# Kernel optimization log

Hardware: AMD Instinct MI355X
Metric: run time of the kernel (lower is better)

## Reference

```python
import jax, jax.numpy as jnp
import numpy as np

NUM_HEADS = 8
GROUP = 16
LN_EPS = 1e-5

def _star_relu(x, scale, bias):
    return scale * jnp.square(jax.nn.relu(x)) + bias

def _layernorm(x, w, b):
    mu = x.mean(-1, keepdims=True)
    var = jnp.mean(jnp.square(x - mu), -1, keepdims=True)
    return (x - mu) / jnp.sqrt(var + LN_EPS) * w + b

def _attention(x, qkv_w, proj_w, proj_b, pa_scale, pa_bias, lf_w, lf_b, hf_w, hf_b, lf_gamma, hf_gamma):
    B, N, C = x.shape
    hd = C // NUM_HEADS
    detail = _star_relu(x, pa_scale, pa_bias)
    lf = jnp.tanh(detail @ lf_w.T + lf_b)                      # (B,N,H)
    hf = jax.nn.softplus(detail @ hf_w.T + hf_b)
    hf_sq = jnp.square(hf)
    hf = 2.0 * hf_sq / (hf_sq + 0.3678)
    lf = jnp.repeat(lf, hd, axis=-1)                           # (B,N,C): per-head value repeated across head_dim
    hf = jnp.repeat(hf, hd, axis=-1)
    qkv = (x @ qkv_w.T).reshape(B, N, 3, NUM_HEADS, hd).transpose(2, 0, 3, 1, 4)
    q, k, v = qkv[0], qkv[1], qkv[2]
    q = q * (hd ** -0.5)
    attn = jax.nn.softmax(jnp.einsum('bhqd,bhkd->bhqk', q, k), axis=-1)
    attn_out = jnp.einsum('bhqk,bhkd->bhqd', attn, v).transpose(0, 2, 1, 3).reshape(B, N, C)
    value_tokens = v.transpose(0, 2, 1, 3).reshape(B, N, C)
    high_res = value_tokens - attn_out
    attn_out = attn_out + attn_out * lf * lf_gamma + hf * high_res * hf_gamma
    return attn_out @ proj_w.T + proj_b

def _freq_scale(x, rw1_w, rw1_scale, rw1_bias, rw2_w, freq_w):
    # x: (B,C,H,W); freq_w: (num_filters, C//group, base_size, base_size//2+1) == rfft grid
    B, C, H, W = x.shape
    xf = jnp.fft.rfft2(x, axes=(2, 3), norm='ortho')           # (B,C,fh,fw) complex
    pooled = x.mean(axis=(2, 3))                               # (B,C)
    h = _star_relu(pooled @ rw1_w.T, rw1_scale, rw1_bias)
    routing = jnp.tanh((h @ rw2_w.T).reshape(B, GROUP, -1))    # (B,g,f)
    fh, fw = xf.shape[2], xf.shape[3]
    dyn = jnp.einsum('bgf,fchw->bgchw', routing, freq_w).reshape(B, C, fh, fw)
    xf = xf * dyn
    return jnp.fft.irfft2(xf, s=(H, W), axes=(2, 3), norm='ortho')

def _forward(x, norm1_w, norm1_b, qkv_w, proj_w, proj_b, pa_scale, pa_bias, lf_w, lf_b, hf_w, hf_b,
             lf_gamma, hf_gamma, fs1_rw1_w, fs1_rw1_scale, fs1_rw1_bias, fs1_rw2_w, fs1_fw, gamma_1,
             norm2_w, norm2_b, fc1_w, fc1_b, fc2_w, fc2_b, fs2_rw1_w, fs2_rw1_scale, fs2_rw1_bias,
             fs2_rw2_w, fs2_fw, gamma_2):
    B, C, H, W = x.shape
    tokens = x.reshape(B, C, H * W).transpose(0, 2, 1)         # nchw -> nlc
    att_tokens = _attention(_layernorm(tokens, norm1_w, norm1_b),
                            qkv_w, proj_w, proj_b, pa_scale, pa_bias,
                            lf_w, lf_b, hf_w, hf_b, lf_gamma, hf_gamma)
    att_feat = att_tokens.transpose(0, 2, 1).reshape(B, C, H, W)
    att_feat = _freq_scale(att_feat, fs1_rw1_w, fs1_rw1_scale, fs1_rw1_bias, fs1_rw2_w, fs1_fw) + att_feat
    att_tokens = att_feat.reshape(B, C, H * W).transpose(0, 2, 1)
    tokens = tokens + gamma_1 * att_tokens
    h = _layernorm(tokens, norm2_w, norm2_b)
    mlp_tokens = jax.nn.gelu(h @ fc1_w.T + fc1_b, approximate=False) @ fc2_w.T + fc2_b
    mlp_feat = mlp_tokens.transpose(0, 2, 1).reshape(B, C, H, W)
    mlp_feat = _freq_scale(mlp_feat, fs2_rw1_w, fs2_rw1_scale, fs2_rw1_bias, fs2_rw2_w, fs2_fw) + mlp_feat
    mlp_tokens = mlp_feat.reshape(B, C, H * W).transpose(0, 2, 1)
    tokens = tokens + gamma_2 * mlp_tokens
    return tokens.transpose(0, 2, 1).reshape(B, C, H, W)

def setup_inputs() -> dict:
    key = jax.random.key(0)
    ks = jax.random.split(key, 16)
    B, C, H, W = 16, 512, 32, 32
    heads, group, nf, bs = 8, 16, 4, 32
    hid_rw = int(C * 0.125)
    hid_mlp = int(C * 4.0)
    bfs = bs // 2 + 1
    d = {}
    d['x'] = jax.random.normal(ks[0], (B, C, H, W), jnp.float32)
    d['norm1_w'] = jnp.ones((C,), jnp.float32); d['norm1_b'] = jnp.zeros((C,), jnp.float32)
    d['qkv_w'] = jax.random.normal(ks[1], (3 * C, C), jnp.float32) * 0.02
    d['proj_w'] = jax.random.normal(ks[2], (C, C), jnp.float32) * 0.02
    d['proj_b'] = jnp.zeros((C,), jnp.float32)
    d['pa_scale'] = jnp.ones((1,), jnp.float32); d['pa_bias'] = jnp.zeros((1,), jnp.float32)
    d['lf_w'] = jax.random.normal(ks[3], (heads, C), jnp.float32) * 0.02
    d['lf_b'] = jnp.zeros((heads,), jnp.float32)
    d['hf_w'] = jax.random.normal(ks[4], (heads, C), jnp.float32) * 0.02
    d['hf_b'] = jnp.zeros((heads,), jnp.float32)
    d['lf_gamma'] = 1e-5 * jnp.ones((C,), jnp.float32)
    d['hf_gamma'] = 1e-5 * jnp.ones((C,), jnp.float32)
    d['fs1_rw1_w'] = jax.random.normal(ks[5], (hid_rw, C), jnp.float32) * 0.02
    d['fs1_rw1_scale'] = jnp.ones((1,), jnp.float32); d['fs1_rw1_bias'] = jnp.zeros((1,), jnp.float32)
    d['fs1_rw2_w'] = jax.random.normal(ks[6], (group * nf, hid_rw), jnp.float32) * 0.02
    d['fs1_fw'] = jax.random.normal(ks[7], (nf, C // group, bs, bfs), jnp.float32) * 1e-5
    d['gamma_1'] = 1e-4 * jnp.ones((C,), jnp.float32)
    d['norm2_w'] = jnp.ones((C,), jnp.float32); d['norm2_b'] = jnp.zeros((C,), jnp.float32)
    d['fc1_w'] = jax.random.normal(ks[8], (hid_mlp, C), jnp.float32) * 0.02
    d['fc1_b'] = jnp.zeros((hid_mlp,), jnp.float32)
    d['fc2_w'] = jax.random.normal(ks[9], (C, hid_mlp), jnp.float32) * 0.02
    d['fc2_b'] = jnp.zeros((C,), jnp.float32)
    d['fs2_rw1_w'] = jax.random.normal(ks[10], (hid_rw, C), jnp.float32) * 0.02
    d['fs2_rw1_scale'] = jnp.ones((1,), jnp.float32); d['fs2_rw1_bias'] = jnp.zeros((1,), jnp.float32)
    d['fs2_rw2_w'] = jax.random.normal(ks[11], (group * nf, hid_rw), jnp.float32) * 0.02
    d['fs2_fw'] = jax.random.normal(ks[12], (nf, C // group, bs, bfs), jnp.float32) * 1e-5
    d['gamma_2'] = 1e-4 * jnp.ones((C,), jnp.float32)
    return d

def reference(x, norm1_w, norm1_b, qkv_w, proj_w, proj_b, pa_scale, pa_bias, lf_w, lf_b, hf_w, hf_b,
              lf_gamma, hf_gamma, fs1_rw1_w, fs1_rw1_scale, fs1_rw1_bias, fs1_rw2_w, fs1_fw, gamma_1,
              norm2_w, norm2_b, fc1_w, fc1_b, fc2_w, fc2_b, fs2_rw1_w, fs2_rw1_scale, fs2_rw1_bias,
              fs2_rw2_w, fs2_fw, gamma_2):
    return _forward(x, norm1_w, norm1_b, qkv_w, proj_w, proj_b, pa_scale, pa_bias, lf_w, lf_b, hf_w, hf_b,
                    lf_gamma, hf_gamma, fs1_rw1_w, fs1_rw1_scale, fs1_rw1_bias, fs1_rw2_w, fs1_fw, gamma_1,
                    norm2_w, norm2_b, fc1_w, fc1_b, fc2_w, fc2_b, fs2_rw1_w, fs2_rw1_scale, fs2_rw1_bias,
                    fs2_rw2_w, fs2_fw, gamma_2)
```

## Files before the change

kernel.cpp:

```cpp
#include <hip/hip_runtime.h>
#include <cstdint>
#include <cstddef>

#define B_   16
#define C_   512
#define N_   1024
#define M_   (B_*N_)
#define NH_  8
#define HD_  64
#define C3_  1536
#define CH_  2048

typedef __attribute__((ext_vector_type(8))) short bf16x8;
typedef __attribute__((ext_vector_type(4))) float f32x4;
typedef __attribute__((ext_vector_type(4))) unsigned short u16x4;

__device__ __forceinline__ unsigned short f2bf(float f) {
  union { float f; unsigned u; } v; v.f = f;
  unsigned r = v.u + 0x7fffu + ((v.u >> 16) & 1u);
  return (unsigned short)(r >> 16);
}
__device__ __forceinline__ float bf2f(unsigned short h) {
  union { unsigned u; float f; } v; v.u = ((unsigned)h) << 16;
  return v.f;
}
__device__ __forceinline__ unsigned f2u(float f) {
  union { float f; unsigned u; } v; v.f = f; return v.u;
}

__global__ __launch_bounds__(256) void k_f2b4(
    const float* __restrict__ s0, unsigned short* __restrict__ d0,
    const float* __restrict__ s1, unsigned short* __restrict__ d1,
    const float* __restrict__ s2, unsigned short* __restrict__ d2,
    const float* __restrict__ s3, unsigned short* __restrict__ d3) {
  int blk = blockIdx.x, t = threadIdx.x;
  const float* s; unsigned short* d; int off;
  if (blk < 3072)      { s = s0; d = d0; off = blk * 256; }
  else if (blk < 4096) { s = s1; d = d1; off = (blk - 3072) * 256; }
  else if (blk < 8192) { s = s2; d = d2; off = (blk - 4096) * 256; }
  else                 { s = s3; d = d3; off = (blk - 8192) * 256; }
  int i = off + t;
  d[i] = f2bf(s[i]);
}

__global__ __launch_bounds__(256) void k_twid(unsigned short* __restrict__ gtab) {
  int idx = blockIdx.x * 256 + threadIdx.x;
  if (idx >= 6400) return;
  int tab = idx / 1280, rem = idx % 1280;
  int i = rem / 40, j = rem % 40;
  float v = 0.f;
  if (j < 32) {
    float th = 0.19634954084936207f * (float)((i * j) & 31);
    float s, c;
    __sincosf(th, &s, &c);
    if (tab == 0) v = c;
    else if (tab == 1) v = s;
    else if (tab == 2) v = -s;
    else {
      float wg = (j == 0 || j == 16) ? 1.f : 2.f;
      if (j >= 17) wg = 0.f;
      v = (tab == 3) ? wg * c : -wg * s;
    }
  }
  gtab[idx] = f2bf(v);
}

template<bool WITH>
__global__ __launch_bounds__(256) void k_lnt(const float* __restrict__ src,
    const float* __restrict__ w, const float* __restrict__ bia,
    const float* __restrict__ lfw, const float* __restrict__ lfb,
    const float* __restrict__ hfw, const float* __restrict__ hfb,
    const float* __restrict__ pa_s, const float* __restrict__ pa_b,
    unsigned short* __restrict__ lnout, float* __restrict__ lfout,
    float* __restrict__ hfout) {
  __shared__ unsigned short s[512 * 34];
  const int t = threadIdx.x, wv = t >> 6, l = t & 63;
  const int n0 = blockIdx.x * 32, b = blockIdx.y;
  const int cl = t >> 3;
  const int nn = (t & 7) * 4;
  #pragma unroll
  for (int k = 0; k < 16; ++k) {
    int c = k * 32 + cl;
    float4 v = *(const float4*)&src[(size_t)(b * C_ + c) * N_ + n0 + nn];
    s[c * 34 + nn]     = f2bf(v.x);
    s[c * 34 + nn + 1] = f2bf(v.y);
    s[c * 34 + nn + 2] = f2bf(v.z);
    s[c * 34 + nn + 3] = f2bf(v.w);
  }
  __syncthreads();
  float wv8[8], bv8[8];
  #pragma unroll
  for (int k = 0; k < 8; ++k) { wv8[k] = w[l + 64 * k]; bv8[k] = bia[l + 64 * k]; }
  float ps = 1.f, pb = 0.f;
  if (WITH) { ps = pa_s[0]; pb = pa_b[0]; }
  for (int ri = 0; ri < 8; ++ri) {
    const int n = wv * 8 + ri;
    const int row = b * N_ + n0 + n;
    float v[8];
    #pragma unroll
    for (int k = 0; k < 8; ++k) v[k] = bf2f(s[(l + 64 * k) * 34 + n]);
    float sm = 0.f, q = 0.f;
    #pragma unroll
    for (int k = 0; k < 8; ++k) { sm += v[k]; q += v[k] * v[k]; }
    #pragma unroll
    for (int off = 1; off < 64; off <<= 1) { sm += __shfl_xor(sm, off); q += __shfl_xor(q, off); }
    float mu = sm * (1.f / 512.f);
    float var = q * (1.f / 512.f) - mu * mu;
    float rstd = rsqrtf(var + 1e-5f);
    float ln[8];
    #pragma unroll
    for (int k = 0; k < 8; ++k) ln[k] = (v[k] - mu) * rstd * wv8[k] + bv8[k];
    #pragma unroll
    for (int k = 0; k < 8; ++k)
      lnout[(size_t)row * C_ + l + 64 * k] = f2bf(ln[k]);
    if (WITH) {
      float d[8];
      #pragma unroll
      for (int k = 0; k < 8; ++k) { float r = fmaxf(ln[k], 0.f); d[k] = ps * r * r + pb; }
      float lacc[8], hacc[8];
      #pragma unroll
      for (int h = 0; h < 8; ++h) {
        float la = 0.f, ha = 0.f;
        #pragma unroll
        for (int k = 0; k < 8; ++k) {
          la += d[k] * lfw[h * C_ + l + 64 * k];
          ha += d[k] * hfw[h * C_ + l + 64 * k];
        }
        lacc[h] = la; hacc[h] = ha;
      }
      #pragma unroll
      for (int h = 0; h < 8; ++h)
        #pragma unroll
        for (int off = 1; off < 64; off <<= 1) {
          lacc[h] += __shfl_xor(lacc[h], off);
          hacc[h] += __shfl_xor(hacc[h], off);
        }
      float lv = lacc[0], hv = hacc[0];
      #pragma unroll
      for (int h = 1; h < 8; ++h) { if (l == h) { lv = lacc[h]; hv = hacc[h]; } }
      if (l < 8) {
        lfout[(size_t)row * 8 + l] = tanhf(lv + lfb[l]);
        float z = hv + hfb[l];
        float sp = (z > 15.f) ? z : log1pf(__expf(z));
        float s2 = sp * sp;
        hfout[(size_t)row * 8 + l] = 2.f * s2 / (s2 + 0.3678f);
      }
    }
  }
}

template<int EPI>
__global__ __launch_bounds__(256) void k_gemm(const unsigned short* __restrict__ A,
    const unsigned short* __restrict__ Bt, const float* __restrict__ bias,
    void* __restrict__ outv, unsigned short* __restrict__ vtg, int Nn, int K) {
  __shared__ __align__(16) unsigned short Asm[128 * 40];
  __shared__ __align__(16) unsigned short Bsm[128 * 40];
  const int t = threadIdx.x, w = t >> 6, l = t & 63;
  const int lane15 = l & 15, quad = l >> 4;
  const int n0 = blockIdx.x * 128, m0 = blockIdx.y * 128;
  const int wm = w >> 1, wn = w & 1;
  f32x4 acc[4][4];
  #pragma unroll
  for (int i = 0; i < 4; ++i)
    #pragma unroll
    for (int j = 0; j < 4; ++j) acc[i][j] = (f32x4){0.f, 0.f, 0.f, 0.f};
  const int sr = t >> 2, sc = (t & 3) * 8;
  const unsigned short* Ab = A + (size_t)(m0 + sr) * K + sc;
  const unsigned short* Bb = Bt + (size_t)(n0 + sr) * K + sc;
  const size_t rstep = (size_t)64 * K;
  bf16x8 ga0 = *(const bf16x8*)Ab;
  bf16x8 ga1 = *(const bf16x8*)(Ab + rstep);
  bf16x8 gb0 = *(const bf16x8*)Bb;
  bf16x8 gb1 = *(const bf16x8*)(Bb + rstep);
  for (int k0 = 0; k0 < K; k0 += 32) {
    __syncthreads();
    *(bf16x8*)&Asm[sr * 40 + sc] = ga0;
    *(bf16x8*)&Asm[(sr + 64) * 40 + sc] = ga1;
    *(bf16x8*)&Bsm[sr * 40 + sc] = gb0;
    *(bf16x8*)&Bsm[(sr + 64) * 40 + sc] = gb1;
    __syncthreads();
    if (k0 + 32 < K) {
      ga0 = *(const bf16x8*)(Ab + k0 + 32);
      ga1 = *(const bf16x8*)(Ab + rstep + k0 + 32);
      gb0 = *(const bf16x8*)(Bb + k0 + 32);
      gb1 = *(const bf16x8*)(Bb + rstep + k0 + 32);
    }
    bf16x8 af[4], bg[4];
    #pragma unroll
    for (int i = 0; i < 4; ++i)
      af[i] = *(const bf16x8*)&Asm[(wm * 64 + i * 16 + lane15) * 40 + quad * 8];
    #pragma unroll
    for (int i = 0; i < 4; ++i)
      bg[i] = *(const bf16x8*)&Bsm[(wn * 64 + i * 16 + lane15) * 40 + quad * 8];
    #pragma unroll
    for (int i = 0; i < 4; ++i)
      #pragma unroll
      for (int j = 0; j < 4; ++j)
        acc[i][j] = __builtin_amdgcn_mfma_f32_16x16x32_bf16(af[i], bg[j], acc[i][j], 0, 0, 0);
  }
  #pragma unroll
  for (int i = 0; i < 4; ++i) {
    int grow = m0 + wm * 64 + i * 16 + quad * 4;
    int bq = grow >> 10, nq = grow & 1023;
    #pragma unroll
    for (int j = 0; j < 4; ++j) {
      int gcol = n0 + wn * 64 + j * 16 + lane15;
      float bs = (EPI == 0) ? 0.f : bias[gcol];
      if (EPI == 1 || EPI == 3) {
        float4 o = make_float4(acc[i][j][0] + bs, acc[i][j][1] + bs,
                               acc[i][j][2] + bs, acc[i][j][3] + bs);
        *(float4*)&((float*)outv)[((size_t)(bq * C_ + gcol) << 10) + nq] = o;
      } else if (EPI == 0) {
        u16x4 pv;
        #pragma unroll
        for (int r = 0; r < 4; ++r) {
          unsigned short hv = f2bf(acc[i][j][r]);
          pv[r] = hv;
          ((unsigned short*)outv)[(size_t)(grow + r) * Nn + gcol] = hv;
        }
        if (gcol >= 1024)
          *(u16x4*)&vtg[((size_t)(bq * C_ + gcol - 1024) << 10) + nq] = pv;
      } else {
        #pragma unroll
        for (int r = 0; r < 4; ++r) {
          float vv = acc[i][j][r] + bs;
          float e = __builtin_amdgcn_exp2f(-(2.302118073f * vv +
                                             0.1029455568f * vv * vv * vv));
          float g = vv * __builtin_amdgcn_rcpf(1.f + e);
          ((unsigned short*)outv)[(size_t)(grow + r) * Nn + gcol] = f2bf(g);
        }
      }
    }
  }
}

__global__ __launch_bounds__(256) void k_flash(const unsigned short* __restrict__ qkv,
    const unsigned short* __restrict__ vtg, const float* __restrict__ lf,
    const float* __restrict__ hf, const float* __restrict__ lgam,
    const float* __restrict__ hgam, unsigned short* __restrict__ y) {
  const int t = threadIdx.x, w = t >> 6, l = t & 63;
  const int lane15 = l & 15, quad = l >> 4;
  const int q0 = blockIdx.x * 64;
  const int h = blockIdx.y, b = blockIdx.z;
  __shared__ __align__(16) unsigned short kt[128 * 72];
  __shared__ __align__(16) unsigned short vt[64 * 136];
  __shared__ __align__(16) unsigned short pl[4][16 * 72];

  bf16x8 aq0, aq1;
  {
    const unsigned short* qp = qkv + (size_t)(b * N_ + q0 + w * 16 + lane15) * C3_ + h * 64 + quad * 8;
    bf16x8 r0 = *(const bf16x8*)qp;
    bf16x8 r1 = *(const bf16x8*)(qp + 32);
    #pragma unroll
    for (int i = 0; i < 8; ++i) {
      aq0[i] = (short)f2bf(0.1803368801111713f * bf2f((unsigned short)r0[i]));
      aq1[i] = (short)f2bf(0.1803368801111713f * bf2f((unsigned short)r1[i]));
    }
  }
  f32x4 O[4];
  #pragma unroll
  for (int i = 0; i < 4; ++i) O[i] = (f32x4){0.f, 0.f, 0.f, 0.f};
  float lsum = 0.f;

  const int sr = t >> 3;
  const int sc = (t & 7) * 8;
  const unsigned short* kb = qkv + (size_t)(b * N_ + sr) * C3_ + 512 + h * 64 + sc;
  const unsigned short* vb = vtg + (size_t)((b * NH_ + h) * HD_ + sr) * N_ + sc;
  bf16x8 gk0 = *(const bf16x8*)kb;
  bf16x8 gk1 = *(const bf16x8*)(kb + (size_t)32 * C3_);
  bf16x8 gk2 = *(const bf16x8*)(kb + (size_t)64 * C3_);
  bf16x8 gk3 = *(const bf16x8*)(kb + (size_t)96 * C3_);
  bf16x8 gv0 = *(const bf16x8*)vb;
  bf16x8 gv1 = *(const bf16x8*)(vb + 64);
  bf16x8 gv2 = *(const bf16x8*)(vb + 32 * N_);
  bf16x8 gv3 = *(const bf16x8*)(vb + 32 * N_ + 64);

  for (int kti = 0; kti < 8; ++kti) {
    __syncthreads();
    *(bf16x8*)&kt[sr * 72 + sc] = gk0;
    *(bf16x8*)&kt[(sr + 32) * 72 + sc] = gk1;
    *(bf16x8*)&kt[(sr + 64) * 72 + sc] = gk2;
    *(bf16x8*)&kt[(sr + 96) * 72 + sc] = gk3;
    *(bf16x8*)&vt[sr * 136 + sc] = gv0;
    *(bf16x8*)&vt[sr * 136 + 64 + sc] = gv1;
    *(bf16x8*)&vt[(sr + 32) * 136 + sc] = gv2;
    *(bf16x8*)&vt[(sr + 32) * 136 + 64 + sc] = gv3;
    __syncthreads();
    if (kti < 7) {
      const unsigned short* kn = kb + (size_t)((kti + 1) * 128) * C3_;
      const unsigned short* vn = vb + (kti + 1) * 128;
      gk0 = *(const bf16x8*)kn;
      gk1 = *(const bf16x8*)(kn + (size_t)32 * C3_);
      gk2 = *(const bf16x8*)(kn + (size_t)64 * C3_);
      gk3 = *(const bf16x8*)(kn + (size_t)96 * C3_);
      gv0 = *(const bf16x8*)vn;
      gv1 = *(const bf16x8*)(vn + 64);
      gv2 = *(const bf16x8*)(vn + 32 * N_);
      gv3 = *(const bf16x8*)(vn + 32 * N_ + 64);
    }

    #pragma unroll
    for (int half = 0; half < 2; ++half) {
      f32x4 S[4];
      #pragma unroll
      for (int nt = 0; nt < 4; ++nt) {
        const int nrow = half * 64 + nt * 16 + lane15;
        bf16x8 ak0 = *(const bf16x8*)&kt[nrow * 72 + quad * 8];
        bf16x8 ak1 = *(const bf16x8*)&kt[nrow * 72 + 32 + quad * 8];
        f32x4 z = (f32x4){0.f, 0.f, 0.f, 0.f};
        z = __builtin_amdgcn_mfma_f32_16x16x32_bf16(ak0, aq0, z, 0, 0, 0);
        z = __builtin_amdgcn_mfma_f32_16x16x32_bf16(ak1, aq1, z, 0, 0, 0);
        S[nt] = z;
      }
      #pragma unroll
      for (int nt = 0; nt < 4; ++nt)
        #pragma unroll
        for (int r = 0; r < 4; ++r) {
          float pv = __builtin_amdgcn_exp2f(S[nt][r]);
          S[nt][r] = pv;
          lsum += pv;
        }
      #pragma unroll
      for (int nt = 0; nt < 4; ++nt) {
        unsigned lo = __builtin_amdgcn_perm(f2u(S[nt][1]), f2u(S[nt][0]), 0x07060302u);
        unsigned hi = __builtin_amdgcn_perm(f2u(S[nt][3]), f2u(S[nt][2]), 0x07060302u);
        uint2 pk = make_uint2(lo, hi);
        *(uint2*)&pl[w][lane15 * 72 + nt * 16 + quad * 4] = pk;
      }
      #pragma unroll
      for (int nc = 0; nc < 2; ++nc) {
        bf16x8 ap = *(const bf16x8*)&pl[w][lane15 * 72 + nc * 32 + quad * 8];
        #pragma unroll
        for (int dt = 0; dt < 4; ++dt) {
          bf16x8 bv = *(const bf16x8*)&vt[(dt * 16 + lane15) * 136 + half * 64 + nc * 32 + quad * 8];
          O[dt] = __builtin_amdgcn_mfma_f32_16x16x32_bf16(ap, bv, O[dt], 0, 0, 0);
        }
      }
    }
  }

  lsum += __shfl_xor(lsum, 16);
  lsum += __shfl_xor(lsum, 32);
  float inv = 1.f / lsum;
  float invr[4], lfr[4], hfr[4];
  #pragma unroll
  for (int r = 0; r < 4; ++r) {
    invr[r] = __shfl(inv, quad * 4 + r);
    int grow = b * N_ + q0 + w * 16 + quad * 4 + r;
    lfr[r] = lf[grow * 8 + h];
    hfr[r] = hf[grow * 8 + h];
  }
  const size_t rowb = (size_t)(b * N_ + q0 + w * 16 + quad * 4);
  #pragma unroll
  for (int dt = 0; dt < 4; ++dt) {
    int cc = h * 64 + dt * 16 + lane15;
    float lg = lgam[cc], hg = hgam[cc];
    #pragma unroll
    for (int r = 0; r < 4; ++r) {
      float a = O[dt][r] * invr[r];
      float vval = bf2f(qkv[(rowb + r) * C3_ + 1024 + cc]);
      float res = a + a * lfr[r] * lg + hfr[r] * (vval - a) * hg;
      y[(rowb + r) * C_ + cc] = f2bf(res);
    }
  }
}

__global__ __launch_bounds__(256) void k_pool(const float* __restrict__ feat,
                                              float* __restrict__ pooled) {
  int row = blockIdx.x * 4 + (threadIdx.x >> 6);
  int l = threadIdx.x & 63;
  const float4* p = (const float4*)(feat + (size_t)row * N_);
  float4 a = p[l], b4 = p[l + 64], c4 = p[l + 128], d4 = p[l + 192];
  float s = a.x + a.y + a.z + a.w + b4.x + b4.y + b4.z + b4.w +
            c4.x + c4.y + c4.z + c4.w + d4.x + d4.y + d4.z + d4.w;
  #pragma unroll
  for (int off = 1; off < 64; off <<= 1) s += __shfl_xor(s, off);
  if (l == 0) pooled[row] = s * (1.f / 1024.f);
}

__global__ __launch_bounds__(256) void k_routing(const float* __restrict__ pooled,
    const float* __restrict__ rw1, const float* __restrict__ rw1s,
    const float* __restrict__ rw1b, const float* __restrict__ rw2,
    float* __restrict__ routing) {
  const int b = blockIdx.x, t = threadIdx.x;
  __shared__ float plds[512];
  __shared__ float tile[64][65];
  __shared__ float hl[64];
  plds[t] = pooled[b * 512 + t];
  plds[t + 256] = pooled[b * 512 + t + 256];
  __syncthreads();
  float acc = 0.f;
  for (int c0 = 0; c0 < 512; c0 += 64) {
    #pragma unroll
    for (int kk = 0; kk < 16; ++kk) {
      int idx = kk * 256 + t;
      tile[idx >> 6][idx & 63] = rw1[(size_t)(idx >> 6) * 512 + c0 + (idx & 63)];
    }
    __syncthreads();
    if (t < 64) {
      #pragma unroll
      for (int i = 0; i < 64; ++i) acc += plds[c0 + i] * tile[t][i];
    }
    __syncthreads();
  }
  if (t < 64) {
    float r = fmaxf(acc, 0.f);
    hl[t] = rw1s[0] * r * r + rw1b[0];
  }
  __syncthreads();
  if (t < 64) {
    float r2 = 0.f;
    #pragma unroll
    for (int j = 0; j < 64; ++j) r2 += hl[j] * rw2[(size_t)t * 64 + j];
    routing[b * 64 + t] = tanhf(r2);
  }
}

__global__ __launch_bounds__(256) void k_freq(const float* __restrict__ feat,
    const float* __restrict__ routing, const float* __restrict__ fwtab,
    const unsigned short* __restrict__ gtab, const float* __restrict__ res,
    const float* __restrict__ gamma, float* __restrict__ outp) {
  const int c = blockIdx.x, b = blockIdx.y, t = threadIdx.x;
  const int g = c >> 5, cc = c & 31;
  const int w = t >> 6, l = t & 63;
  const int lane15 = l & 15, quad = l >> 4;
  const int mt = w & 1, nt = w >> 1;
  __shared__ __align__(16) unsigned short Xbf[32 * 40];
  __shared__ __align__(16) float p[32 * 36];
  __shared__ __align__(16) unsigned short Tabs[6400];
  __shared__ __align__(16) unsigned short pl1r[32 * 40], pl1i[32 * 40];
  __shared__ __align__(16) unsigned short pl2r[32 * 40], pl2i[32 * 40];
  __shared__ __align__(16) unsigned short pl3r[32 * 40], pl3i[32 * 40];
  __shared__ float Ms[1024];
  const size_t base = (size_t)(b * C_ + c) * N_;

  {
    float4 v = ((const float4*)(feat + base))[t];
    int hh = t >> 3, w4 = (t & 7) * 4;
    *(float4*)&p[hh * 36 + w4] = v;
    u16x4 xb = { f2bf(v.x), f2bf(v.y), f2bf(v.z), f2bf(v.w) };
    *(u16x4*)&Xbf[hh * 40 + w4] = xb;
  }
  {
    const uint4* src = (const uint4*)gtab;
    uint4* dst = (uint4*)Tabs;
    #pragma unroll
    for (int k = 0; k < 4; ++k) {
      int o = k * 256 + t;
      if (o < 800) dst[o] = src[o];
    }
  }
  {
    float r0 = routing[b * 64 + g * 4 + 0];
    float r1 = routing[b * 64 + g * 4 + 1];
    float r2 = routing[b * 64 + g * 4 + 2];
    float r3 = routing[b * 64 + g * 4 + 3];
    const float* fb = fwtab + (size_t)cc * 544;
    #pragma unroll
    for (int k = 0; k < 4; ++k) {
      int o = k * 256 + t;
      int fh = o >> 5, fw = o & 31;
      float mv = 0.f;
      if (fw < 17) {
        int fi = fh * 17 + fw;
        mv = (r0 * fb[fi] + r1 * fb[17408 + fi] + r2 * fb[34816 + fi] +
              r3 * fb[52224 + fi]) * (1.f / 1024.f);
      }
      Ms[o] = mv;
    }
  }
  __syncthreads();

  const unsigned short* Tc  = Tabs;
  const unsigned short* Ts  = Tabs + 1280;
  const unsigned short* Tsn = Tabs + 2560;
  const unsigned short* Tcw = Tabs + 3840;
  const unsigned short* Tsw = Tabs + 5120;
  const int arow = (mt * 16 + lane15) * 40 + quad * 8;
  const int brow = (nt * 16 + lane15) * 40 + quad * 8;
  const int prow = (nt * 16 + lane15) * 40 + mt * 16 + quad * 4;
  const f32x4 zz = (f32x4){0.f, 0.f, 0.f, 0.f};

  {
    bf16x8 aX = *(const bf16x8*)&Xbf[arow];
    bf16x8 bC = *(const bf16x8*)&Tc[brow];
    bf16x8 bS = *(const bf16x8*)&Tsn[brow];
    f32x4 re = __builtin_amdgcn_mfma_f32_16x16x32_bf16(aX, bC, zz, 0, 0, 0);
    f32x4 im = __builtin_amdgcn_mfma_f32_16x16x32_bf16(aX, bS, zz, 0, 0, 0);
    uint2 pr = make_uint2(__builtin_amdgcn_perm(f2u(re[1]), f2u(re[0]), 0x07060302u),
                          __builtin_amdgcn_perm(f2u(re[3]), f2u(re[2]), 0x07060302u));
    uint2 pi = make_uint2(__builtin_amdgcn_perm(f2u(im[1]), f2u(im[0]), 0x07060302u),
                          __builtin_amdgcn_perm(f2u(im[3]), f2u(im[2]), 0x07060302u));
    *(uint2*)&pl1r[prow] = pr;
    *(uint2*)&pl1i[prow] = pi;
  }
  __syncthreads();
  {
    bf16x8 aC = *(const bf16x8*)&Tc[arow];
    bf16x8 aS = *(const bf16x8*)&Ts[arow];
    bf16x8 aN = *(const bf16x8*)&Tsn[arow];
    bf16x8 bR = *(const bf16x8*)&pl1r[brow];
    bf16x8 bI = *(const bf16x8*)&pl1i[brow];
    f32x4 er = __builtin_amdgcn_mfma_f32_16x16x32_bf16(aC, bR, zz, 0, 0, 0);
    er = __builtin_amdgcn_mfma_f32_16x16x32_bf16(aS, bI, er, 0, 0, 0);
    f32x4 ei = __builtin_amdgcn_mfma_f32_16x16x32_bf16(aC, bI, zz, 0, 0, 0);
    ei = __builtin_amdgcn_mfma_f32_16x16x32_bf16(aN, bR, ei, 0, 0, 0);
    #pragma unroll
    for (int r = 0; r < 4; ++r) {
      float mk = Ms[(mt * 16 + quad * 4 + r) * 32 + nt * 16 + lane15];
      er[r] *= mk; ei[r] *= mk;
    }
    uint2 pr = make_uint2(__builtin_amdgcn_perm(f2u(er[1]), f2u(er[0]), 0x07060302u),
                          __builtin_amdgcn_perm(f2u(er[3]), f2u(er[2]), 0x07060302u));
    uint2 pi = make_uint2(__builtin_amdgcn_perm(f2u(ei[1]), f2u(ei[0]), 0x07060302u),
                          __builtin_amdgcn_perm(f2u(ei[3]), f2u(ei[2]), 0x07060302u));
    *(uint2*)&pl2r[prow] = pr;
    *(uint2*)&pl2i[prow] = pi;
  }
  __syncthreads();
  {
    bf16x8 aR = *(const bf16x8*)&pl2r[arow];
    bf16x8 aI = *(const bf16x8*)&pl2i[arow];
    bf16x8 bC = *(const bf16x8*)&Tc[brow];
    bf16x8 bS = *(const bf16x8*)&Ts[brow];
    bf16x8 bN = *(const bf16x8*)&Tsn[brow];
    f32x4 zr = __builtin_amdgcn_mfma_f32_16x16x32_bf16(aR, bC, zz, 0, 0, 0);
    zr = __builtin_amdgcn_mfma_f32_16x16x32_bf16(aI, bN, zr, 0, 0, 0);
    f32x4 zi = __builtin_amdgcn_mfma_f32_16x16x32_bf16(aI, bC, zz, 0, 0, 0);
    zi = __builtin_amdgcn_mfma_f32_16x16x32_bf16(aR, bS, zi, 0, 0, 0);
    uint2 pr = make_uint2(__builtin_amdgcn_perm(f2u(zr[1]), f2u(zr[0]), 0x07060302u),
                          __builtin_amdgcn_perm(f2u(zr[3]), f2u(zr[2]), 0x07060302u));
    uint2 pi = make_uint2(__builtin_amdgcn_perm(f2u(zi[1]), f2u(zi[0]), 0x07060302u),
                          __builtin_amdgcn_perm(f2u(zi[3]), f2u(zi[2]), 0x07060302u));
    *(uint2*)&pl3r[prow] = pr;
    *(uint2*)&pl3i[prow] = pi;
  }
  __syncthreads();
  {
    bf16x8 aC = *(const bf16x8*)&Tcw[arow];
    bf16x8 aS = *(const bf16x8*)&Tsw[arow];
    bf16x8 bR = *(const bf16x8*)&pl3r[brow];
    bf16x8 bI = *(const bf16x8*)&pl3i[brow];
    f32x4 y = __builtin_amdgcn_mfma_f32_16x16x32_bf16(aC, bR, zz, 0, 0, 0);
    y = __builtin_amdgcn_mfma_f32_16x16x32_bf16(aS, bI, y, 0, 0, 0);
    int hh = nt * 16 + lane15, w0 = mt * 16 + quad * 4;
    float4 fp = *(const float4*)&p[hh * 36 + w0];
    float4 rp = *(const float4*)&res[base + hh * 32 + w0];
    float gv = gamma[c];
    float4 o = make_float4(rp.x + gv * (y[0] + fp.x), rp.y + gv * (y[1] + fp.y),
                           rp.z + gv * (y[2] + fp.z), rp.w + gv * (y[3] + fp.w));
    *(float4*)&outp[base + hh * 32 + w0] = o;
  }
}

extern "C" void kernel_launch(void* const* d_in, const int* in_sizes, int n_in,
                              void* d_out, int out_size, void* d_ws, size_t ws_size,
                              hipStream_t stream) {
  (void)in_sizes; (void)n_in; (void)out_size; (void)ws_size;
  const float* x      = (const float*)d_in[0];
  const float* n1w    = (const float*)d_in[1];
  const float* n1b    = (const float*)d_in[2];
  const float* qkv_w  = (const float*)d_in[3];
  const float* proj_w = (const float*)d_in[4];
  const float* proj_b = (const float*)d_in[5];
  const float* pa_s   = (const float*)d_in[6];
  const float* pa_b   = (const float*)d_in[7];
  const float* lf_w   = (const float*)d_in[8];
  const float* lf_b   = (const float*)d_in[9];
  const float* hf_w   = (const float*)d_in[10];
  const float* hf_b   = (const float*)d_in[11];
  const float* lf_g   = (const float*)d_in[12];
  const float* hf_g   = (const float*)d_in[13];
  const float* f1rw1w = (const float*)d_in[14];
  const float* f1rw1s = (const float*)d_in[15];
  const float* f1rw1b = (const float*)d_in[16];
  const float* f1rw2w = (const float*)d_in[17];
  const float* f1fw   = (const float*)d_in[18];
  const float* gamma1 = (const float*)d_in[19];
  const float* n2w    = (const float*)d_in[20];
  const float* n2b    = (const float*)d_in[21];
  const float* fc1w   = (const float*)d_in[22];
  const float* fc1b   = (const float*)d_in[23];
  const float* fc2w   = (const float*)d_in[24];
  const float* fc2b   = (const float*)d_in[25];
  const float* f2rw1w = (const float*)d_in[26];
  const float* f2rw1s = (const float*)d_in[27];
  const float* f2rw1b = (const float*)d_in[28];
  const float* f2rw2w = (const float*)d_in[29];
  const float* f2fw   = (const float*)d_in[30];
  const float* gamma2 = (const float*)d_in[31];

  char* ws = (char*)d_ws;
  float*          tokens = (float*)(ws + 0);
  float*          f1buf  = (float*)(ws + 33554432ULL);
  float*          f2buf  = (float*)(ws + 67108864ULL);
  unsigned short* regA   = (unsigned short*)(ws + 134217728ULL);
  unsigned short* abuf   = (unsigned short*)(ws + 201326592ULL);
  float*          lfbuf  = (float*)(ws + 218103808ULL);
  float*          hfbuf  = (float*)(ws + 218628096ULL);
  float*          pooled = (float*)(ws + 219152384ULL);
  float*          routing= (float*)(ws + 219185152ULL);
  unsigned short* wq     = (unsigned short*)(ws + 219189248ULL);
  unsigned short* wp     = (unsigned short*)(ws + 220762112ULL);
  unsigned short* w1     = (unsigned short*)(ws + 221286400ULL);
  unsigned short* w2     = (unsigned short*)(ws + 223383552ULL);
  unsigned short* gtab   = (unsigned short*)(ws + 225480704ULL);
  unsigned short* vtg    = (unsigned short*)f1buf;

  k_f2b4<<<12288, 256, 0, stream>>>(qkv_w, wq, proj_w, wp, fc1w, w1, fc2w, w2);
  k_twid<<<25, 256, 0, stream>>>(gtab);

  k_lnt<true><<<dim3(32, 16), 256, 0, stream>>>(x, n1w, n1b, lf_w, lf_b, hf_w, hf_b,
                                                pa_s, pa_b, abuf, lfbuf, hfbuf);
  k_gemm<0><<<dim3(12, 128), 256, 0, stream>>>(abuf, wq, n1b, regA, vtg, C3_, C_);
  k_flash<<<dim3(16, 8, 16), 256, 0, stream>>>(regA, vtg, lfbuf, hfbuf, lf_g, hf_g, abuf);
  k_gemm<1><<<dim3(4, 128), 256, 0, stream>>>(abuf, wp, proj_b, f2buf, nullptr, C_, C_);
  k_pool<<<2048, 256, 0, stream>>>(f2buf, pooled);
  k_routing<<<16, 256, 0, stream>>>(pooled, f1rw1w, f1rw1s, f1rw1b, f1rw2w, routing);
  k_freq<<<dim3(512, 16), 256, 0, stream>>>(f2buf, routing, f1fw, gtab, x, gamma1, tokens);
  k_lnt<false><<<dim3(32, 16), 256, 0, stream>>>(tokens, n2w, n2b, nullptr, nullptr,
                                                 nullptr, nullptr, nullptr, nullptr,
                                                 abuf, nullptr, nullptr);
  k_gemm<2><<<dim3(16, 128), 256, 0, stream>>>(abuf, w1, fc1b, regA, nullptr, CH_, C_);
  k_gemm<3><<<dim3(4, 128), 256, 0, stream>>>(regA, w2, fc2b, f2buf, nullptr, C_, CH_);
  k_pool<<<2048, 256, 0, stream>>>(f2buf, pooled);
  k_routing<<<16, 256, 0, stream>>>(pooled, f2rw1w, f2rw1s, f2rw1b, f2rw2w, routing);
  k_freq<<<dim3(512, 16), 256, 0, stream>>>(f2buf, routing, f2fw, gtab, tokens, gamma2,
                                            (float*)d_out);
}
```

Before: 519.1 us.

## Use direct global-to-LDS loads and XCD-aware block remapping in GEMM and flash attention

GEMM and flash-attention tile staging now uses global_load_lds, which writes global data straight into LDS instead of going through registers. The LDS padding is replaced by unpadded tiles, with an XOR swizzle in flash attention. Blocks are remapped with XCD-aware ordering so neighbouring tiles share an L2. Flash now processes 128 queries per block with 64-key tiles, uses s_setprio around MFMA sections and sets occupancy bounds. The register prefetch double-buffering is removed, so load latency is no longer overlapped, and the unpadded GEMM LDS layout may cause bank conflicts.

```diff
diff --git a/kernel.cpp b/kernel.cpp
--- a/kernel.cpp
+++ b/kernel.cpp
@@ -27,6 +27,11 @@
 __device__ __forceinline__ unsigned f2u(float f) {
   union { float f; unsigned u; } v; v.f = f; return v.u;
 }
+
+#define GL16(gp, lp) \
+  __builtin_amdgcn_global_load_lds( \
+      (const __attribute__((address_space(1))) unsigned int*)(const void*)(gp), \
+      (__attribute__((address_space(3))) unsigned int*)(void*)(lp), 16, 0, 0)
 
 __global__ __launch_bounds__(256) void k_f2b4(
     const float* __restrict__ s0, unsigned short* __restrict__ d0,
@@ -152,46 +157,44 @@
 template<int EPI>
 __global__ __launch_bounds__(256) void k_gemm(const unsigned short* __restrict__ A,
     const unsigned short* __restrict__ Bt, const float* __restrict__ bias,
-    void* __restrict__ outv, unsigned short* __restrict__ vtg, int Nn, int K) {
-  __shared__ __align__(16) unsigned short Asm[128 * 40];
-  __shared__ __align__(16) unsigned short Bsm[128 * 40];
+    void* __restrict__ outv, unsigned short* __restrict__ vtg, int Nn, int K, int nx) {
+  __shared__ __align__(16) unsigned short Asm[128 * 32];
+  __shared__ __align__(16) unsigned short Bsm[128 * 32];
   const int t = threadIdx.x, w = t >> 6, l = t & 63;
   const int lane15 = l & 15, quad = l >> 4;
-  const int n0 = blockIdx.x * 128, m0 = blockIdx.y * 128;
+  const int cpx = gridDim.x >> 3;
+  const int wgs = (blockIdx.x & 7) * cpx + (blockIdx.x >> 3);
+  const int bx = wgs % nx, by = wgs / nx;
+  const int n0 = bx * 128, m0 = by * 128;
   const int wm = w >> 1, wn = w & 1;
   f32x4 acc[4][4];
   #pragma unroll
   for (int i = 0; i < 4; ++i)
     #pragma unroll
     for (int j = 0; j < 4; ++j) acc[i][j] = (f32x4){0.f, 0.f, 0.f, 0.f};
-  const int sr = t >> 2, sc = (t & 3) * 8;
-  const unsigned short* Ab = A + (size_t)(m0 + sr) * K + sc;
-  const unsigned short* Bb = Bt + (size_t)(n0 + sr) * K + sc;
-  const size_t rstep = (size_t)64 * K;
-  bf16x8 ga0 = *(const bf16x8*)Ab;
-  bf16x8 ga1 = *(const bf16x8*)(Ab + rstep);
-  bf16x8 gb0 = *(const bf16x8*)Bb;
-  bf16x8 gb1 = *(const bf16x8*)(Bb + rstep);
+  const int srow = w * 16 + (l >> 2);
+  const int scol = (l & 3) * 8;
+  const unsigned short* gA = A + (size_t)(m0 + srow) * K + scol;
+  const unsigned short* gB = Bt + (size_t)(n0 + srow) * K + scol;
+  const size_t rk64 = (size_t)64 * K;
+  char* lA0 = (char*)Asm + w * 1024;
+  char* lA1 = (char*)Asm + 4096 + w * 1024;
+  char* lB0 = (char*)Bsm + w * 1024;
+  char* lB1 = (char*)Bsm + 4096 + w * 1024;
   for (int k0 = 0; k0 < K; k0 += 32) {
     __syncthreads();
-    *(bf16x8*)&Asm[sr * 40 + sc] = ga0;
-    *(bf16x8*)&Asm[(sr + 64) * 40 + sc] = ga1;
-    *(bf16x8*)&Bsm[sr * 40 + sc] = gb0;
-    *(bf16x8*)&Bsm[(sr + 64) * 40 + sc] = gb1;
+    GL16(gA + k0, lA0);
+    GL16(gA + k0 + rk64, lA1);
+    GL16(gB + k0, lB0);
+    GL16(gB + k0 + rk64, lB1);
     __syncthreads();
-    if (k0 + 32 < K) {
-      ga0 = *(const bf16x8*)(Ab + k0 + 32);
-      ga1 = *(const bf16x8*)(Ab + rstep + k0 + 32);
-      gb0 = *(const bf16x8*)(Bb + k0 + 32);
-      gb1 = *(const bf16x8*)(Bb + rstep + k0 + 32);
-    }
     bf16x8 af[4], bg[4];
     #pragma unroll
     for (int i = 0; i < 4; ++i)
-      af[i] = *(const bf16x8*)&Asm[(wm * 64 + i * 16 + lane15) * 40 + quad * 8];
+      af[i] = *(const bf16x8*)&Asm[(wm * 64 + i * 16 + lane15) * 32 + quad * 8];
     #pragma unroll
     for (int i = 0; i < 4; ++i)
-      bg[i] = *(const bf16x8*)&Bsm[(wn * 64 + i * 16 + lane15) * 40 + quad * 8];
+      bg[i] = *(const bf16x8*)&Bsm[(wn * 64 + i * 16 + lane15) * 32 + quad * 8];
     #pragma unroll
     for (int i = 0; i < 4; ++i)
       #pragma unroll
@@ -234,133 +237,131 @@
   }
 }
 
-__global__ __launch_bounds__(256) void k_flash(const unsigned short* __restrict__ qkv,
+__global__ __launch_bounds__(256, 4) void k_flash(const unsigned short* __restrict__ qkv,
     const unsigned short* __restrict__ vtg, const float* __restrict__ lf,
     const float* __restrict__ hf, const float* __restrict__ lgam,
     const float* __restrict__ hgam, unsigned short* __restrict__ y) {
   const int t = threadIdx.x, w = t >> 6, l = t & 63;
   const int lane15 = l & 15, quad = l >> 4;
-  const int q0 = blockIdx.x * 64;
-  const int h = blockIdx.y, b = blockIdx.z;
-  __shared__ __align__(16) unsigned short kt[128 * 72];
-  __shared__ __align__(16) unsigned short vt[64 * 136];
+  const int wg = (blockIdx.x & 7) * 128 + (blockIdx.x >> 3);
+  const int qt = wg & 7;
+  const int h = (wg >> 3) & 7;
+  const int b = wg >> 6;
+  const int q0 = qt * 128;
+
+  __shared__ __align__(16) unsigned short kt[64 * 64];
+  __shared__ __align__(16) unsigned short vt[64 * 64];
   __shared__ __align__(16) unsigned short pl[4][16 * 72];
 
-  bf16x8 aq0, aq1;
-  {
-    const unsigned short* qp = qkv + (size_t)(b * N_ + q0 + w * 16 + lane15) * C3_ + h * 64 + quad * 8;
+  bf16x8 aq[2][2];
+  #pragma unroll
+  for (int qh = 0; qh < 2; ++qh) {
+    const unsigned short* qp = qkv +
+        (size_t)(b * N_ + q0 + w * 32 + qh * 16 + lane15) * C3_ + h * 64 + quad * 8;
     bf16x8 r0 = *(const bf16x8*)qp;
     bf16x8 r1 = *(const bf16x8*)(qp + 32);
     #pragma unroll
     for (int i = 0; i < 8; ++i) {
-      aq0[i] = (short)f2bf(0.1803368801111713f * bf2f((unsigned short)r0[i]));
-      aq1[i] = (short)f2bf(0.1803368801111713f * bf2f((unsigned short)r1[i]));
-    }
-  }
-  f32x4 O[4];
-  #pragma unroll
-  for (int i = 0; i < 4; ++i) O[i] = (f32x4){0.f, 0.f, 0.f, 0.f};
-  float lsum = 0.f;
-
-  const int sr = t >> 3;
-  const int sc = (t & 7) * 8;
-  const unsigned short* kb = qkv + (size_t)(b * N_ + sr) * C3_ + 512 + h * 64 + sc;
-  const unsigned short* vb = vtg + (size_t)((b * NH_ + h) * HD_ + sr) * N_ + sc;
-  bf16x8 gk0 = *(const bf16x8*)kb;
-  bf16x8 gk1 = *(const bf16x8*)(kb + (size_t)32 * C3_);
-  bf16x8 gk2 = *(const bf16x8*)(kb + (size_t)64 * C3_);
-  bf16x8 gk3 = *(const bf16x8*)(kb + (size_t)96 * C3_);
-  bf16x8 gv0 = *(const bf16x8*)vb;
-  bf16x8 gv1 = *(const bf16x8*)(vb + 64);
-  bf16x8 gv2 = *(const bf16x8*)(vb + 32 * N_);
-  bf16x8 gv3 = *(const bf16x8*)(vb + 32 * N_ + 64);
-
-  for (int kti = 0; kti < 8; ++kti) {
+      aq[qh][0][i] = (short)f2bf(0.1803368801111713f * bf2f((unsigned short)r0[i]));
+      aq[qh][1][i] = (short)f2bf(0.1803368801111713f * bf2f((unsigned short)r1[i]));
+    }
+  }
+  f32x4 O[2][4];
+  #pragma unroll
+  for (int qh = 0; qh < 2; ++qh)
+    #pragma unroll
+    for (int i = 0; i < 4; ++i) O[qh][i] = (f32x4){0.f, 0.f, 0.f, 0.f};
+  float lsum[2] = {0.f, 0.f};
+
+  const int prow = w * 8 + (l >> 3);
+  const int csw = ((l & 7) ^ (l >> 3)) * 8;
+  const unsigned short* kg = qkv + (size_t)(b * N_ + prow) * C3_ + 512 + h * 64 + csw;
+  const unsigned short* vg = vtg + (size_t)((b * NH_ + h) * HD_ + prow) * N_ + csw;
+  char* ktb0 = (char*)kt + w * 1024;
+  char* ktb1 = (char*)kt + 4096 + w * 1024;
+  char* vtb0 = (char*)vt + w * 1024;
+  char* vtb1 = (char*)vt + 4096 + w * 1024;
+  const int swx = (lane15 & 7) * 8;
+
+  for (int kti = 0; kti < 16; ++kti) {
     __syncthreads();
-    *(bf16x8*)&kt[sr * 72 + sc] = gk0;
-    *(bf16x8*)&kt[(sr + 32) * 72 + sc] = gk1;
-    *(bf16x8*)&kt[(sr + 64) * 72 + sc] = gk2;
-    *(bf16x8*)&kt[(sr + 96) * 72 + sc] = gk3;
-    *(bf16x8*)&vt[sr * 136 + sc] = gv0;
-    *(bf16x8*)&vt[sr * 136 + 64 + sc] = gv1;
-    *(bf16x8*)&vt[(sr + 32) * 136 + sc] = gv2;
-    *(bf16x8*)&vt[(sr + 32) * 136 + 64 + sc] = gv3;
+    const unsigned short* kr = kg + (size_t)(kti * 64) * C3_;
+    GL16(kr, ktb0);
+    GL16(kr + (size_t)32 * C3_, ktb1);
+    const unsigned short* vr = vg + kti * 64;
+    GL16(vr, vtb0);
+    GL16(vr + 32 * N_, vtb1);
     __syncthreads();
-    if (kti < 7) {
-      const unsigned short* kn = kb + (size_t)((kti + 1) * 128) * C3_;
-      const unsigned short* vn = vb + (kti + 1) * 128;
-      gk0 = *(const bf16x8*)kn;
-      gk1 = *(const bf16x8*)(kn + (size_t)32 * C3_);
-      gk2 = *(const bf16x8*)(kn + (size_t)64 * C3_);
-      gk3 = *(const bf16x8*)(kn + (size_t)96 * C3_);
-      gv0 = *(const bf16x8*)vn;
-      gv1 = *(const bf16x8*)(vn + 64);
-      gv2 = *(const bf16x8*)(vn + 32 * N_);
-      gv3 = *(const bf16x8*)(vn + 32 * N_ + 64);
-    }
-
-    #pragma unroll
-    for (int half = 0; half < 2; ++half) {
+
+    #pragma unroll
+    for (int qh = 0; qh < 2; ++qh) {
       f32x4 S[4];
+      __builtin_amdgcn_s_setprio(1);
       #pragma unroll
       for (int nt = 0; nt < 4; ++nt) {
-        const int nrow = half * 64 + nt * 16 + lane15;
-        bf16x8 ak0 = *(const bf16x8*)&kt[nrow * 72 + quad * 8];
-        bf16x8 ak1 = *(const bf16x8*)&kt[nrow * 72 + 32 + quad * 8];
+        const int nrow = nt * 16 + lane15;
+        bf16x8 ak0 = *(const bf16x8*)&kt[nrow * 64 + ((quad * 8) ^ swx)];
+        bf16x8 ak1 = *(const bf16x8*)&kt[nrow * 64 + ((32 + quad * 8) ^ swx)];
         f32x4 z = (f32x4){0.f, 0.f, 0.f, 0.f};
-        z = __builtin_amdgcn_mfma_f32_16x16x32_bf16(ak0, aq0, z, 0, 0, 0);
-        z = __builtin_amdgcn_mfma_f32_16x16x32_bf16(ak1, aq1, z, 0, 0, 0);
+        z = __builtin_amdgcn_mfma_f32_16x16x32_bf16(ak0, aq[qh][0], z, 0, 0, 0);
+        z = __builtin_amdgcn_mfma_f32_16x16x32_bf16(ak1, aq[qh][1], z, 0, 0, 0);
         S[nt] = z;
       }
+      __builtin_amdgcn_s_setprio(0);
       #pragma unroll
       for (int nt = 0; nt < 4; ++nt)
         #pragma unroll
         for (int r = 0; r < 4; ++r) {
           float pv = __builtin_amdgcn_exp2f(S[nt][r]);
           S[nt][r] = pv;
-          lsum += pv;
+          lsum[qh] += pv;
         }
       #pragma unroll
       for (int nt = 0; nt < 4; ++nt) {
         unsigned lo = __builtin_amdgcn_perm(f2u(S[nt][1]), f2u(S[nt][0]), 0x07060302u);
         unsigned hi = __builtin_amdgcn_perm(f2u(S[nt][3]), f2u(S[nt][2]), 0x07060302u);
-        uint2 pk = make_uint2(lo, hi);
-        *(uint2*)&pl[w][lane15 * 72 + nt * 16 + quad * 4] = pk;
-      }
+        *(uint2*)&pl[w][lane15 * 72 + nt * 16 + quad * 4] = make_uint2(lo, hi);
+      }
+      __builtin_amdgcn_s_setprio(1);
       #pragma unroll
       for (int nc = 0; nc < 2; ++nc) {
         bf16x8 ap = *(const bf16x8*)&pl[w][lane15 * 72 + nc * 32 + quad * 8];
         #pragma unroll
         for (int dt = 0; dt < 4; ++dt) {
-          bf16x8 bv = *(const bf16x8*)&vt[(dt * 16 + lane15) * 136 + half * 64 + nc * 32 + quad * 8];
-          O[dt] = __builtin_amdgcn_mfma_f32_16x16x32_bf16(ap, bv, O[dt], 0, 0, 0);
+          const int vrow = dt * 16 + lane15;
+          bf16x8 bv = *(const bf16x8*)&vt[vrow * 64 + ((nc * 32 + quad * 8) ^ swx)];
+          O[qh][dt] = __builtin_amdgcn_mfma_f32_16x16x32_bf16(ap, bv, O[qh][dt], 0, 0, 0);
         }
       }
-    }
-  }
-
-  lsum += __shfl_xor(lsum, 16);
-  lsum += __shfl_xor(lsum, 32);
-  float inv = 1.f / lsum;
-  float invr[4], lfr[4], hfr[4];
-  #pragma unroll
-  for (int r = 0; r < 4; ++r) {
-    invr[r] = __shfl(inv, quad * 4 + r);
-    int grow = b * N_ + q0 + w * 16 + quad * 4 + r;
-    lfr[r] = lf[grow * 8 + h];
-    hfr[r] = hf[grow * 8 + h];
-  }
-  const size_t rowb = (size_t)(b * N_ + q0 + w * 16 + quad * 4);
-  #pragma unroll
-  for (int dt = 0; dt < 4; ++dt) {
-    int cc = h * 64 + dt * 16 + lane15;
-    float lg = lgam[cc], hg = hgam[cc];
+      __builtin_amdgcn_s_setprio(0);
+    }
+  }
+
+  #pragma unroll
+  for (int qh = 0; qh < 2; ++qh) {
+    float s = lsum[qh];
+    s += __shfl_xor(s, 16);
+    s += __shfl_xor(s, 32);
+    float inv = 1.f / s;
+    float invr[4], lfr[4], hfr[4];
+    const size_t rowb = (size_t)(b * N_ + q0 + w * 32 + qh * 16 + quad * 4);
     #pragma unroll
     for (int r = 0; r < 4; ++r) {
-      float a = O[dt][r] * invr[r];
-      float vval = bf2f(qkv[(rowb + r) * C3_ + 1024 + cc]);
-      float res = a + a * lfr[r] * lg + hfr[r] * (vval - a) * hg;
-      y[(rowb + r) * C_ + cc] = f2bf(res);
+      invr[r] = __shfl(inv, quad * 4 + r);
+      lfr[r] = lf[(rowb + r) * 8 + h];
+      hfr[r] = hf[(rowb + r) * 8 + h];
+    }
+    #pragma unroll
+    for (int dt = 0; dt < 4; ++dt) {
+      const int cc = h * 64 + dt * 16 + lane15;
+      const float lg = lgam[cc], hg = hgam[cc];
+      #pragma unroll
+      for (int r = 0; r < 4; ++r) {
+        float a = O[qh][dt][r] * invr[r];
+        float vval = bf2f(qkv[(rowb + r) * C3_ + 1024 + cc]);
+        float res = a + a * lfr[r] * lg + hfr[r] * (vval - a) * hg;
+        y[(rowb + r) * C_ + cc] = f2bf(res);
+      }
     }
   }
 }
@@ -612,17 +613,17 @@
 
   k_lnt<true><<<dim3(32, 16), 256, 0, stream>>>(x, n1w, n1b, lf_w, lf_b, hf_w, hf_b,
                                                 pa_s, pa_b, abuf, lfbuf, hfbuf);
-  k_gemm<0><<<dim3(12, 128), 256, 0, stream>>>(abuf, wq, n1b, regA, vtg, C3_, C_);
-  k_flash<<<dim3(16, 8, 16), 256, 0, stream>>>(regA, vtg, lfbuf, hfbuf, lf_g, hf_g, abuf);
-  k_gemm<1><<<dim3(4, 128), 256, 0, stream>>>(abuf, wp, proj_b, f2buf, nullptr, C_, C_);
+  k_gemm<0><<<1536, 256, 0, stream>>>(abuf, wq, n1b, regA, vtg, C3_, C_, 12);
+  k_flash<<<1024, 256, 0, stream>>>(regA, vtg, lfbuf, hfbuf, lf_g, hf_g, abuf);
+  k_gemm<1><<<512, 256, 0, stream>>>(abuf, wp, proj_b, f2buf, nullptr, C_, C_, 4);
   k_pool<<<2048, 256, 0, stream>>>(f2buf, pooled);
   k_routing<<<16, 256, 0, stream>>>(pooled, f1rw1w, f1rw1s, f1rw1b, f1rw2w, routing);
   k_freq<<<dim3(512, 16), 256, 0, stream>>>(f2buf, routing, f1fw, gtab, x, gamma1, tokens);
   k_lnt<false><<<dim3(32, 16), 256, 0, stream>>>(tokens, n2w, n2b, nullptr, nullptr,
                                                  nullptr, nullptr, nullptr, nullptr,
                                                  abuf, nullptr, nullptr);
-  k_gemm<2><<<dim3(16, 128), 256, 0, stream>>>(abuf, w1, fc1b, regA, nullptr, CH_, C_);
-  k_gemm<3><<<dim3(4, 128), 256, 0, stream>>>(regA, w2, fc2b, f2buf, nullptr, C_, CH_);
+  k_gemm<2><<<2048, 256, 0, stream>>>(abuf, w1, fc1b, regA, nullptr, CH_, C_, 16);
+  k_gemm<3><<<512, 256, 0, stream>>>(regA, w2, fc2b, f2buf, nullptr, C_, CH_, 4);
   k_pool<<<2048, 256, 0, stream>>>(f2buf, pooled);
   k_routing<<<16, 256, 0, stream>>>(pooled, f2rw1w, f2rw1s, f2rw1b, f2rw2w, routing);
   k_freq<<<dim3(512, 16), 256, 0, stream>>>(f2buf, routing, f2fw, gtab, tokens, gamma2,
```

After: 513.2 us. Within noise of the previous version (-1.1%).
